# Optimization experiments

Measured on AMD Instinct MI355X. Metric: run time of the kernel, lower is better.

The kernel has to match this reference:

```python
import jax, jax.numpy as jnp
import numpy as np

V, E, H, T = 50000, 256, 512, 9
B, S = 128, 512
HD = H // 2  # per-direction LSTM hidden


def _lstm_dir(x, w_ih, w_hh, b_ih, b_hh):
    # x: [B,S,E]; PyTorch gate order i,f,g,o
    xg = jnp.einsum('bse,ge->bsg', x, w_ih) + b_ih + b_hh  # [B,S,4*HD]
    b = x.shape[0]
    h0 = jnp.zeros((b, HD), x.dtype)
    c0 = jnp.zeros((b, HD), x.dtype)

    def step(carry, xt):
        h, c = carry
        g = xt + h @ w_hh.T
        i, f, gg, o = jnp.split(g, 4, axis=-1)
        c = jax.nn.sigmoid(f) * c + jax.nn.sigmoid(i) * jnp.tanh(gg)
        h = jax.nn.sigmoid(o) * jnp.tanh(c)
        return (h, c), h

    _, hs = jax.lax.scan(step, (h0, c0), jnp.swapaxes(xg, 0, 1))
    return jnp.swapaxes(hs, 0, 1)  # [B,S,HD]


def _crf_llh(emissions, y, mask, start_trans, end_trans, trans):
    # emissions [B,S,T], y [B,S] int, mask [B,S] bool -> scalar sum LLH
    em = jnp.swapaxes(emissions, 0, 1)  # [S,B,T]
    ys = jnp.swapaxes(y, 0, 1)          # [S,B]
    mf = jnp.swapaxes(mask, 0, 1).astype(emissions.dtype)  # [S,B]
    b = emissions.shape[0]
    bidx = jnp.arange(b)

    # --- numerator: gold path score ---
    score0 = start_trans[ys[0]] + em[0, bidx, ys[0]]

    def num_step(carry, inp):
        score, yp = carry
        e_t, y_t, m_t = inp
        s = trans[yp, y_t] + e_t[bidx, y_t]
        score = score + s * m_t
        yp = jnp.where(m_t > 0, y_t, yp)
        return (score, yp), None

    (score, ylast), _ = jax.lax.scan(num_step, (score0, ys[0]),
                                     (em[1:], ys[1:], mf[1:]))
    numerator = score + end_trans[ylast]

    # --- denominator: forward algorithm ---
    alpha0 = start_trans + em[0]  # [B,T]

    def den_step(alpha, inp):
        e_t, m_t = inp
        nxt = jax.nn.logsumexp(alpha[:, :, None] + trans[None] + e_t[:, None, :], axis=1)
        return jnp.where(m_t[:, None] > 0, nxt, alpha), None

    alpha, _ = jax.lax.scan(den_step, alpha0, (em[1:], mf[1:]))
    denominator = jax.nn.logsumexp(alpha + end_trans, axis=1)
    return jnp.sum(numerator - denominator)


def setup_inputs() -> dict:
    key = jax.random.key(0)
    ks = jax.random.split(key, 16)
    X = jax.random.randint(ks[0], (B, S), 0, V)
    y = jax.random.randint(ks[1], (B, S), 0, T)
    lengths = jax.random.randint(ks[2], (B,), S // 2, S + 1)
    mask = jnp.arange(S)[None, :] < lengths[:, None]  # contiguous, mask[:,0]=True
    s = 0.1
    emb = jax.random.normal(ks[3], (V, E), jnp.float32)
    w_ih_f = jax.random.normal(ks[4], (4 * HD, E), jnp.float32) * s
    w_hh_f = jax.random.normal(ks[5], (4 * HD, HD), jnp.float32) * s
    b_ih_f = jnp.zeros((4 * HD,), jnp.float32)
    b_hh_f = jnp.zeros((4 * HD,), jnp.float32)
    w_ih_b = jax.random.normal(ks[6], (4 * HD, E), jnp.float32) * s
    w_hh_b = jax.random.normal(ks[7], (4 * HD, HD), jnp.float32) * s
    b_ih_b = jnp.zeros((4 * HD,), jnp.float32)
    b_hh_b = jnp.zeros((4 * HD,), jnp.float32)
    lin_w = jax.random.normal(ks[8], (T, H), jnp.float32) * s
    lin_b = jnp.zeros((T,), jnp.float32)
    start_trans = jax.random.uniform(ks[9], (T,), jnp.float32, -0.1, 0.1)
    end_trans = jax.random.uniform(ks[10], (T,), jnp.float32, -0.1, 0.1)
    trans = jax.random.uniform(ks[11], (T, T), jnp.float32, -0.1, 0.1)
    return dict(X=X, y=y, mask=mask, emb=emb,
                w_ih_f=w_ih_f, w_hh_f=w_hh_f, b_ih_f=b_ih_f, b_hh_f=b_hh_f,
                w_ih_b=w_ih_b, w_hh_b=w_hh_b, b_ih_b=b_ih_b, b_hh_b=b_hh_b,
                lin_w=lin_w, lin_b=lin_b,
                start_trans=start_trans, end_trans=end_trans, trans=trans)


def reference(X, y, mask, emb,
              w_ih_f, w_hh_f, b_ih_f, b_hh_f,
              w_ih_b, w_hh_b, b_ih_b, b_hh_b,
              lin_w, lin_b, start_trans, end_trans, trans):
    x = emb[X]  # [B,S,E]
    h_f = _lstm_dir(x, w_ih_f, w_hh_f, b_ih_f, b_hh_f)
    h_b = _lstm_dir(x[:, ::-1, :], w_ih_b, w_hh_b, b_ih_b, b_hh_b)[:, ::-1, :]
    o = jnp.concatenate([h_f, h_b], axis=-1)  # [B,S,H]
    emissions = jnp.einsum('bsh,th->bst', o, lin_w) + lin_b  # [B,S,T]
    return _crf_llh(emissions, y, mask, start_trans, end_trans, trans)
```

## Files before the change

kernel.cpp:

```cpp
#include <hip/hip_runtime.h>


typedef short v8s __attribute__((ext_vector_type(8)));
typedef float v4f __attribute__((ext_vector_type(4)));
typedef int   i4v __attribute__((ext_vector_type(4)));
typedef int   i8v __attribute__((ext_vector_type(8)));
typedef float v2f __attribute__((ext_vector_type(2)));

#define LOG2E  1.4426950408889634f
#define LOG2E2 2.8853900817779268f

__device__ __forceinline__ short f2b(float f){
  unsigned u = __float_as_uint(f);
  u = u + 0x7fffu + ((u >> 16) & 1u);
  return (short)(u >> 16);
}
__device__ __forceinline__ float b2f(short s){
  return __uint_as_float(((unsigned)(unsigned short)s) << 16);
}
__device__ __forceinline__ float rcp_(float x){ return __builtin_amdgcn_rcpf(x); }
__device__ __forceinline__ float ex2(float x){ return __builtin_amdgcn_exp2f(x); }
__device__ __forceinline__ float med3(float x, float lo, float hi){
  return __builtin_amdgcn_fmed3f(x, lo, hi);
}
__device__ __forceinline__ float selq(v4f v, int q){
  return q==0 ? v[0] : q==1 ? v[1] : q==2 ? v[2] : v[3];
}
__device__ __forceinline__ int fp4q(float v){
  int s = (v < 0.f) ? 8 : 0;
  float av = fabsf(v);
  int m;
  if(av < 0.25f) m=0; else if(av < 0.75f) m=1; else if(av < 1.25f) m=2;
  else if(av < 1.75f) m=3; else if(av < 2.5f) m=4; else if(av < 3.5f) m=5;
  else if(av < 5.f) m=6; else m=7;
  return s | m;
}

__global__ void prep_kernel(const float* wihf, const float* whhf,
                            const float* wihb, const float* whhb,
                            const float* bihf, const float* bhhf,
                            const float* bihb, const float* bhhb,
                            short* wswz, unsigned char* whh4, int2* whsc,
                            float* cb, float* em, float* outp)
{
  int gid = blockIdx.x * 256 + threadIdx.x;
  if(gid < 65536){
    int mat = gid >> 15;
    int rem = gid & 32767;
    int ct = rem >> 9;
    int kk = (rem >> 6) & 7;
    int lane = rem & 63;
    const float* src = mat ? wihb : wihf;
    int g  = ct*16 + (lane & 15);
    float fac = ((g >> 8) == 2) ? LOG2E2 : LOG2E;
    int k0 = kk*32 + (lane >> 4)*8;
    v8s o;
#pragma unroll
    for(int j=0;j<8;j++) o[j] = f2b(src[g*256 + k0 + j] * fac);
    *(v8s*)(wswz + ((long)mat << 18) + ((long)((ct*8+kk)*64 + lane) << 3)) = o;
  } else if(gid < 73728){
    int j2 = gid - 65536;
    int dir = j2 >> 12;
    int rem = j2 & 4095;
    int ct = rem >> 6;
    int lane = rem & 63;
    const float* src = dir ? whhb : whhf;
    int g = ct*16 + (lane & 15);
    float fac = ((g >> 8) == 2) ? LOG2E2 : LOG2E;
    int sc0 = 127, sc1 = 127;
#pragma unroll
    for(int half=0; half<2; half++){
      const float* s = src + g*256 + half*128 + (lane>>4)*32;
      float am = 0.f;
#pragma unroll
      for(int j=0;j<32;j++) am = fmaxf(am, fabsf(s[j]*fac));
      int e = 0;
      if(am > 0.f){
        e = (int)ceilf(log2f(am * (1.f/6.f)));
        e = e < -126 ? -126 : (e > 127 ? 127 : e);
      }
      float inv = exp2f((float)(-e)) * fac;
      i4v ov;
#pragma unroll
      for(int wi=0; wi<4; wi++){
        int word = 0;
#pragma unroll
        for(int bj=0; bj<4; bj++){
          int j0 = (wi*4 + bj)*2;
          int c0 = fp4q(s[j0]*inv), c1 = fp4q(s[j0+1]*inv);
          word |= (c0 | (c1<<4)) << (8*bj);
        }
        ov[wi] = word;
      }
      *(i4v*)(whh4 + ((long)((dir*64+ct)*2 + half) << 10) + lane*16) = ov;
      if(half == 0) sc0 = e + 127; else sc1 = e + 127;
    }
    whsc[(dir*64+ct)*64 + lane] = make_int2(sc0, sc1);
  } else if(gid >= 106496 && gid < 108544){
    int j3 = gid - 106496;
    int dir = j3 >> 10, gg = j3 & 1023;
    float fac = ((gg >> 8) == 2) ? LOG2E2 : LOG2E;
    cb[j3] = fac * (dir ? (bihb[gg] + bhhb[gg]) : (bihf[gg] + bhhf[gg]));
  }
  for(int i=gid; i<589824; i+=131072) em[i] = 0.f;
  if(gid == 0) *outp = 0.f;
}

__global__ __launch_bounds__(256,2) void xg_gemm(const int* X, const float* emb,
     const short* wswz, const float* cb, short* xg, int t_base, int CT)
{
  int dir = blockIdx.x & 1;
  int tl  = blockIdx.x >> 1;
  int rh  = blockIdx.y;
  int tg  = t_base + tl;
  int tt  = dir ? (511 - tg) : tg;
  __shared__ short a_sh[64*264];
  int tid = threadIdx.x;
  {
    int row = tid >> 2, seg = tid & 3;
    int b = rh*64 + row;
    int idx = X[b*512 + tt];
    const float* erow = emb + (long)idx*256 + seg*64;
    short* dst = a_sh + row*264 + seg*64;
#pragma unroll
    for(int c=0;c<8;c++){
      float4 f0 = ((const float4*)erow)[2*c];
      float4 f1 = ((const float4*)erow)[2*c+1];
      v8s p;
      p[0]=f2b(f0.x); p[1]=f2b(f0.y); p[2]=f2b(f0.z); p[3]=f2b(f0.w);
      p[4]=f2b(f1.x); p[5]=f2b(f1.y); p[6]=f2b(f1.z); p[7]=f2b(f1.w);
      *(v8s*)(dst + c*8) = p;
    }
  }
  __syncthreads();
  int w = tid >> 6, lane = tid & 63, lm = lane & 15, lq = lane >> 4;
  v8s A[4][8];
#pragma unroll
  for(int mt=0;mt<4;mt++)
#pragma unroll
    for(int kk=0;kk<8;kk++)
      A[mt][kk] = *(const v8s*)(a_sh + (mt*16+lm)*264 + kk*32 + lq*8);

  const short* wmat = wswz + ((long)dir << 18);
  const float* cbd  = cb + dir*1024;
  short* xgd = xg + ((long)dir*CT + tl)*131072;

  v8s Bb[2][8];
  {
    const short* bp = wmat + (long)(w*16)*4096 + lane*8;
#pragma unroll
    for(int kk=0;kk<8;kk++) Bb[0][kk] = *(const v8s*)(bp + kk*512);
  }
#pragma unroll
  for(int ci=0;ci<16;ci++){
    int cur = ci & 1;
    int ct = w*16 + ci;
    if(ci < 15){
      const short* bp = wmat + (long)(ct+1)*4096 + lane*8;
#pragma unroll
      for(int kk=0;kk<8;kk++) Bb[cur^1][kk] = *(const v8s*)(bp + kk*512);
    }
    float bias = cbd[ct*16 + lm];
    v4f acc[4];
#pragma unroll
    for(int mt=0;mt<4;mt++) acc[mt] = (v4f){bias,bias,bias,bias};
#pragma unroll
    for(int kk=0;kk<8;kk++)
#pragma unroll
      for(int mt=0;mt<4;mt++)
        acc[mt] = __builtin_amdgcn_mfma_f32_16x16x32_bf16(A[mt][kk], Bb[cur][kk], acc[mt], 0,0,0);
#pragma unroll
    for(int mt=0;mt<4;mt++){
      int r = rh*4 + mt;
      long off = (long)r*16384 + (long)(ct & 15)*1024 + (ct >> 4)*256 + lane*4;
      short4 s4;
      s4.x = f2b(acc[mt][0]); s4.y = f2b(acc[mt][1]);
      s4.z = f2b(acc[mt][2]); s4.w = f2b(acc[mt][3]);
      *(short4*)(xgd + off) = s4;
    }
  }
}

__global__ void emiss_partial(const unsigned char* hg8, const float* lin_w,
                              float* em, int t_base, int CT)
{
  int dir = blockIdx.y;
  int wv  = blockIdx.x*4 + (threadIdx.x >> 6);
  int lane = threadIdx.x & 63;
  int tl = wv >> 7, b = wv & 127;
  int s = dir ? (511 - (t_base + tl)) : (t_base + tl);
  int v = *(const int*)(hg8 + ((long)dir*CT + tl)*32768 + b*256 + lane*4);
  v2f lo = __builtin_amdgcn_cvt_pk_f32_fp8(v, 0);
  v2f hi = __builtin_amdgcn_cvt_pk_f32_fp8(v, 1);
  float x0 = lo[0], x1 = lo[1], x2 = hi[0], x3 = hi[1];
  const float* wbase = lin_w + dir*256 + lane*4;
  float part[9];
#pragma unroll
  for(int j=0;j<9;j++){
    float4 wf = *(const float4*)(wbase + j*512);
    part[j] = x0*wf.x + x1*wf.y + x2*wf.z + x3*wf.w;
  }
#pragma unroll
  for(int j=0;j<9;j++){
    float vv = part[j];
#pragma unroll
    for(int off=32; off>0; off>>=1) vv += __shfl_down(vv, off);
    if(lane == 0) em[((long)b*512 + s)*9 + j] += vv;
  }
}

__global__ __launch_bounds__(1024,1) void fused_step(
     const int* __restrict__ X, const float* __restrict__ emb,
     const short* __restrict__ wswz, const float* __restrict__ cb,
     const short* __restrict__ xg_rd, short* __restrict__ xg_wr,
     const unsigned char* __restrict__ whh4, const int2* __restrict__ whsc,
     unsigned char* __restrict__ hg_wr, const unsigned char* __restrict__ hg_rd,
     float* __restrict__ c_state, unsigned char* __restrict__ h_state,
     const float* __restrict__ lin_w, float* __restrict__ em,
     int first, int CT, int tb_gemm, int tb_emiss, int ng)
{
  __shared__ __align__(16) short a_sh4[4*16*264];
  int bx = blockIdx.x;
  int tid = threadIdx.x;

  if(bx < 64){
    unsigned char* hbuf = (unsigned char*)a_sh4;
    int wg = bx;
    int dir = wg >> 5, rg = wg & 31;
    int w = tid >> 6, lane = tid & 63, lm = lane & 15, lq = lane >> 4;
    int lr = lm & 3;

    i8v B8[4][2];
#pragma unroll
    for(int grp=0; grp<4; grp++)
#pragma unroll
      for(int half=0; half<2; half++){
        i4v b = *(const i4v*)(whh4 + ((long)((dir*64 + grp*16 + w)*2 + half) << 10) + lane*16);
        i8v t;
#pragma unroll
        for(int j=0;j<4;j++){ t[j] = b[j]; t[4+j] = 0; }
        B8[grp][half] = t;
      }
    int scp[2];
#pragma unroll
    for(int gp=0; gp<2; gp++){
      int2 s0 = whsc[(dir*64 + (2*gp+0)*16 + w)*64 + lane];
      int2 s1 = whsc[(dir*64 + (2*gp+1)*16 + w)*64 + lane];
      scp[gp] = (s0.x & 255) | ((s0.y & 255) << 8) | ((s1.x & 255) << 16) | ((s1.y & 255) << 24);
    }

    for(int i=tid; i<8704; i+=1024) hbuf[i] = 0;
    float c = first ? 0.f : c_state[wg*1024 + tid];
    __syncthreads();
    if(!first && tid < 256){
      int row = tid >> 6, col = tid & 63;
      *(int*)(hbuf + row*272 + col*4) = *(const int*)(h_state + wg*1024 + row*256 + col*4);
    }
    __syncthreads();

    const short* __restrict__ xbase =
        xg_rd + ((long)dir*CT)*131072 + (long)(rg >> 2)*16384 + w*1024 + ((rg & 3)*16 + lm)*4;
    int hrow = tid >> 6, hcol = tid & 63;
    unsigned char* __restrict__ houtb =
        hg_wr + (long)dir*CT*32768 + (rg*4 + hrow)*256 + hcol*4;

    short4 xa0 = *(const short4*)(xbase);
    short4 xa1 = *(const short4*)(xbase + 256);
    short4 xa2 = *(const short4*)(xbase + 512);
    short4 xa3 = *(const short4*)(xbase + 768);

    int p = 0;
    for(int tl=0; tl<CT; tl++){
      const short* __restrict__ xn = xbase + 131072;
      short4 xn0 = *(const short4*)(xn);
      short4 xn1 = *(const short4*)(xn + 256);
      short4 xn2 = *(const short4*)(xn + 512);
      short4 xn3 = *(const short4*)(xn + 768);

      const unsigned char* hb = hbuf + p*4352;
      union { i8v v8; i4v v4[2]; } a0, a1;
      a0.v4[0] = *(const i4v*)(hb + lr*272 + lq*32);
      a0.v4[1] = *(const i4v*)(hb + lr*272 + lq*32 + 16);
      a1.v4[0] = *(const i4v*)(hb + lr*272 + 128 + lq*32);
      a1.v4[1] = *(const i4v*)(hb + lr*272 + 128 + lq*32 + 16);

      v4f acc[4];
      acc[0] = (v4f){b2f(xa0.x), b2f(xa0.y), b2f(xa0.z), b2f(xa0.w)};
      acc[1] = (v4f){b2f(xa1.x), b2f(xa1.y), b2f(xa1.z), b2f(xa1.w)};
      acc[2] = (v4f){b2f(xa2.x), b2f(xa2.y), b2f(xa2.z), b2f(xa2.w)};
      acc[3] = (v4f){b2f(xa3.x), b2f(xa3.y), b2f(xa3.z), b2f(xa3.w)};

      acc[0] = __builtin_amdgcn_mfma_scale_f32_16x16x128_f8f6f4(a0.v8, B8[0][0], acc[0], 0, 4, 0, 127, 0, scp[0]);
      acc[0] = __builtin_amdgcn_mfma_scale_f32_16x16x128_f8f6f4(a1.v8, B8[0][1], acc[0], 0, 4, 0, 127, 1, scp[0]);
      acc[1] = __builtin_amdgcn_mfma_scale_f32_16x16x128_f8f6f4(a0.v8, B8[1][0], acc[1], 0, 4, 0, 127, 2, scp[0]);
      acc[1] = __builtin_amdgcn_mfma_scale_f32_16x16x128_f8f6f4(a1.v8, B8[1][1], acc[1], 0, 4, 0, 127, 3, scp[0]);
      acc[2] = __builtin_amdgcn_mfma_scale_f32_16x16x128_f8f6f4(a0.v8, B8[2][0], acc[2], 0, 4, 0, 127, 0, scp[1]);
      acc[2] = __builtin_amdgcn_mfma_scale_f32_16x16x128_f8f6f4(a1.v8, B8[2][1], acc[2], 0, 4, 0, 127, 1, scp[1]);
      acc[3] = __builtin_amdgcn_mfma_scale_f32_16x16x128_f8f6f4(a0.v8, B8[3][0], acc[3], 0, 4, 0, 127, 2, scp[1]);
      acc[3] = __builtin_amdgcn_mfma_scale_f32_16x16x128_f8f6f4(a1.v8, B8[3][1], acc[3], 0, 4, 0, 127, 3, scp[1]);

      float g0 = selq(acc[0], lq);
      float g1 = selq(acc[1], lq);
      float g2 = selq(acc[2], lq);
      float g3 = selq(acc[3], lq);

      unsigned char* hnew = hbuf + (p^1)*4352;
      {
        float ig = g0;
        float fg = g1;
        float gg = med3(g2, -40.f, 40.f);
        float og = g3;
        float t  = ex2(gg);
        float a  = ex2(-ig);
        float b  = ex2(-fg);
        float u  = ex2(-og);
        float term = (t - 1.f) * rcp_((1.f + a)*(1.f + t));
        float cn = c*rcp_(1.f + b) + term;
        c = cn;
        float cc = med3(cn*LOG2E2, -40.f, 40.f);
        float d2 = ex2(cc);
        float hv = (d2 - 1.f)*rcp_((1.f + u)*(1.f + d2));
        int packed = __builtin_amdgcn_cvt_pk_fp8_f32(hv, hv, 0, 0);
        hnew[lq*272 + 16*w + lm] = (unsigned char)(packed & 0xff);
      }
      __syncthreads();
      if(tid < 256)
        *(int*)houtb = *(const int*)(hnew + hrow*272 + hcol*4);
      houtb += 32768;
      xbase += 131072;
      xa0 = xn0; xa1 = xn1; xa2 = xn2; xa3 = xn3;
      p ^= 1;
    }
    {
      const unsigned char* hb = hbuf + p*4352;
      if(tid < 256)
        *(int*)(h_state + wg*1024 + hrow*256 + hcol*4) = *(const int*)(hb + hrow*272 + hcol*4);
      c_state[wg*1024 + tid] = c;
    }

  } else if(bx < 64 + ng){
    int q = tid >> 8;
    int t256 = tid & 255;
    int u = (bx - 64)*4 + q;
    int dir = u & 1;
    int v = u >> 1;
    int tl = v % CT;
    int rgh = v / CT;
    int tg = tb_gemm + tl;
    int tt = dir ? (511 - tg) : tg;
    short* a_shq = a_sh4 + q*4224;
    int w2 = t256 >> 6, lane = t256 & 63, lm = lane & 15, lq = lane >> 4;
    const short* wmat = wswz + ((long)dir << 18);
    const float* cbd  = cb + dir*1024;
    short* xgd = xg_wr + ((long)dir*CT + tl)*131072;

    for(int it=0; it<4; it++){
      int rg = rgh*4 + it;
      {
        int row = t256 >> 4, seg = t256 & 15;
        int b = rg*16 + row;
        int idx = X[b*512 + tt];
        const float* erow = emb + (long)idx*256 + seg*16;
        float4 f0 = ((const float4*)erow)[0];
        float4 f1 = ((const float4*)erow)[1];
        float4 f2 = ((const float4*)erow)[2];
        float4 f3 = ((const float4*)erow)[3];
        v8s p0, p1;
        p0[0]=f2b(f0.x); p0[1]=f2b(f0.y); p0[2]=f2b(f0.z); p0[3]=f2b(f0.w);
        p0[4]=f2b(f1.x); p0[5]=f2b(f1.y); p0[6]=f2b(f1.z); p0[7]=f2b(f1.w);
        p1[0]=f2b(f2.x); p1[1]=f2b(f2.y); p1[2]=f2b(f2.z); p1[3]=f2b(f2.w);
        p1[4]=f2b(f3.x); p1[5]=f2b(f3.y); p1[6]=f2b(f3.z); p1[7]=f2b(f3.w);
        *(v8s*)(a_shq + row*264 + seg*16) = p0;
        *(v8s*)(a_shq + row*264 + seg*16 + 8) = p1;
      }
      __syncthreads();
      v8s A[8];
#pragma unroll
      for(int kk=0;kk<8;kk++)
        A[kk] = *(const v8s*)(a_shq + lm*264 + kk*32 + lq*8);

#pragma unroll 1
      for(int ci=0; ci<16; ci++){
        int ct = w2*16 + ci;
        const short* bp = wmat + (long)ct*4096 + lane*8;
        v8s Bb[8];
#pragma unroll
        for(int kk=0;kk<8;kk++) Bb[kk] = *(const v8s*)(bp + kk*512);
        float bias = cbd[ct*16 + lm];
        v4f acc = (v4f){bias,bias,bias,bias};
#pragma unroll
        for(int kk=0;kk<8;kk++)
          acc = __builtin_amdgcn_mfma_f32_16x16x32_bf16(A[kk], Bb[kk], acc, 0,0,0);
        long off = (long)rg*16384 + (long)(ct & 15)*1024 + (ct >> 4)*256 + lane*4;
        short4 s4;
        s4.x = f2b(acc[0]); s4.y = f2b(acc[1]);
        s4.z = f2b(acc[2]); s4.w = f2b(acc[3]);
        *(short4*)(xgd + off) = s4;
      }
      __syncthreads();
    }

  } else {
    int uv = (bx - 64 - ng)*16 + (tid >> 6);
    int lane = tid & 63;
    int per = CT << 7;
    int dir = (uv >= per) ? 1 : 0;
    int rest = uv - (dir ? per : 0);
    int tl = rest >> 7, b = rest & 127;
    int s = dir ? (511 - (tb_emiss + tl)) : (tb_emiss + tl);
    int v = *(const int*)(hg_rd + ((long)dir*CT + tl)*32768 + b*256 + lane*4);
    v2f lo = __builtin_amdgcn_cvt_pk_f32_fp8(v, 0);
    v2f hi = __builtin_amdgcn_cvt_pk_f32_fp8(v, 1);
    float x0 = lo[0], x1 = lo[1], x2 = hi[0], x3 = hi[1];
    const float* wbase = lin_w + dir*256 + lane*4;
    float part[9];
#pragma unroll
    for(int j=0;j<9;j++){
      float4 wf = *(const float4*)(wbase + j*512);
      part[j] = x0*wf.x + x1*wf.y + x2*wf.z + x3*wf.w;
    }
#pragma unroll
    for(int j=0;j<9;j++){
      float vv = part[j];
#pragma unroll
      for(int off=32; off>0; off>>=1) vv += __shfl_down(vv, off);
      if(lane == 0) em[((long)b*512 + s)*9 + j] += vv;
    }
  }
}

__global__ __launch_bounds__(64) void crf_kernel(
                           const float* em, const int* y, const unsigned char* maskb,
                           const float* st, const float* en, const float* tr,
                           const float* lin_b, float* out)
{
  __shared__ __align__(16) float ems[4608];
  int b = blockIdx.x;
  int lane = threadIdx.x;

  {
    const float4* src = (const float4*)(em + (long)b*4608);
    float4* dst = (float4*)ems;
    for(int i = lane; i < 1152; i += 64) dst[i] = src[i];
  }

  bool isb = (maskb[1] != 0);
  int len = 0;
  for(int k=lane; k<512; k+=64){
    unsigned char mv = isb ? maskb[b*512 + k] : maskb[((long)(b*512 + k))*4];
    len += (mv != 0);
  }
#pragma unroll
  for(int off=32; off>0; off>>=1) len += __shfl_xor(len, off);

  __syncthreads();

  const int* yb = y + b*512;
  float np = 0.f;
  for(int t=lane; t<512; t+=64){
    if(t >= 1 && t < len){
      int yp = yb[t-1], yt = yb[t];
      np += tr[yp*9 + yt] + ems[t*9 + yt] + lin_b[yt];
    }
  }
#pragma unroll
  for(int off=32; off>0; off>>=1) np += __shfl_xor(np, off);

  int j = lane;
  float alpha = -1e30f;
  float trc[9];
  float lb = (j < 9) ? lin_b[j] : 0.f;
  if(j < 9){
    alpha = st[j] + ems[j] + lb;
#pragma unroll
    for(int i=0;i<9;i++) trc[i] = tr[i*9 + j];
  }
  for(int t=1; t<len; t++){
    float av[9];
#pragma unroll
    for(int i=0;i<9;i++) av[i] = __shfl(alpha, i);
    if(j < 9){
      float m = av[0] + trc[0];
#pragma unroll
      for(int i=1;i<9;i++) m = fmaxf(m, av[i] + trc[i]);
      float ssum = 0.f;
#pragma unroll
      for(int i=0;i<9;i++) ssum += __expf(av[i] + trc[i] - m);
      alpha = m + __logf(ssum) + ems[t*9 + j] + lb;
    }
  }
  float aj = (j < 9) ? (alpha + en[j]) : -1e30f;
  float mm = aj;
#pragma unroll
  for(int off=32; off>0; off>>=1) mm = fmaxf(mm, __shfl_xor(mm, off));
  float ee = (j < 9) ? __expf(aj - mm) : 0.f;
#pragma unroll
  for(int off=32; off>0; off>>=1) ee += __shfl_xor(ee, off);
  float den = mm + __logf(ee);
  if(lane == 0){
    int y0 = yb[0];
    float num = np + st[y0] + ems[y0] + lin_b[y0] + en[yb[len-1]];
    atomicAdd(out, num - den);
  }
}

extern "C" void kernel_launch(void* const* d_in, const int* in_sizes, int n_in,
                              void* d_out, int out_size, void* d_ws, size_t ws_size,
                              hipStream_t stream)
{
  (void)in_sizes; (void)n_in; (void)out_size;
  const int*   X    = (const int*)d_in[0];
  const int*   y    = (const int*)d_in[1];
  const unsigned char* maskb = (const unsigned char*)d_in[2];
  const float* emb  = (const float*)d_in[3];
  const float* wihf = (const float*)d_in[4];
  const float* whhf = (const float*)d_in[5];
  const float* bihf = (const float*)d_in[6];
  const float* bhhf = (const float*)d_in[7];
  const float* wihb = (const float*)d_in[8];
  const float* whhb = (const float*)d_in[9];
  const float* bihb = (const float*)d_in[10];
  const float* bhhb = (const float*)d_in[11];
  const float* lin_w= (const float*)d_in[12];
  const float* lin_b= (const float*)d_in[13];
  const float* st   = (const float*)d_in[14];
  const float* en   = (const float*)d_in[15];
  const float* tr   = (const float*)d_in[16];

  const long FIXED = 4595712L;
  long CT = 128;
  while (CT > 16 && FIXED + 2*CT*589824L > (long)ws_size) CT >>= 1;
  int NC = (int)(512 / CT);

  char* ws = (char*)d_ws;
  short*         wswz = (short*)(ws);
  unsigned char* whh4 = (unsigned char*)(ws + 1572864L);
  int2*          whsc = (int2*)(ws + 1835008L);
  float*         cb   = (float*)(ws + 1900544L);
  float*         cst  = (float*)(ws + 1908736L);
  unsigned char* hst  = (unsigned char*)(ws + 2170880L);
  float*         em   = (float*)(ws + 2236416L);
  short*         xg0  = (short*)(ws + FIXED);
  short*         xg1  = xg0 + CT*262144;
  unsigned char* hg0  = (unsigned char*)(ws + FIXED + 2*CT*524288L);
  unsigned char* hg1  = hg0 + CT*65536;

  prep_kernel<<<512, 256, 0, stream>>>(wihf, whhf, wihb, whhb,
                                       bihf, bhhf, bihb, bhhb,
                                       wswz, whh4, whsc, cb, em, (float*)d_out);
  xg_gemm<<<dim3(2*(int)CT, 2), 256, 0, stream>>>(X, emb, wswz, cb, xg0, 0, (int)CT);

  for(int k=0; k<NC; k++){
    short* xr = (k&1) ? xg1 : xg0;
    short* xw = (k&1) ? xg0 : xg1;
    unsigned char* hw = (k&1) ? hg1 : hg0;
    unsigned char* hr = (k&1) ? hg0 : hg1;
    int ng = (k+1 < NC) ? (int)CT : 0;
    int ne = (k >= 1)   ? (int)(16*CT) : 0;
    fused_step<<<64 + ng + ne, 1024, 0, stream>>>(
        X, emb, wswz, cb, xr, xw, whh4, whsc, hw, hr, cst, hst, lin_w, em,
        (k==0) ? 1 : 0, (int)CT, (k+1)*(int)CT, (k-1)*(int)CT, ng);
  }
  unsigned char* hlast = ((NC-1)&1) ? hg1 : hg0;
  emiss_partial<<<dim3(32*(int)CT, 2), 256, 0, stream>>>(hlast, lin_w, em, (NC-1)*(int)CT, (int)CT);
  crf_kernel<<<128, 64, 0, stream>>>(em, y, maskb, st, en, tr, lin_b, (float*)d_out);
}
```

Measured before the change: 816.2 us.

## Rewrite CRF forward pass as per-thread exp-domain matvec with precomputed exp(trans)

Splits the CRF kernel into numerator blocks and two denominator blocks, in which each thread runs the whole forward algorithm for one batch row. The denominator works in the exp domain: exp(trans + lin_b) is precomputed once in prep, so each step is one max, 9 exp2, an 81-FMA matvec and 9 log2, with no cross-lane shuffles and no shared-memory staging. It aims to shorten the serial dependency chain of the latency-bound recurrence. In exchange, each thread always runs all 511 steps and masks them instead of stopping at its length, emission reads are strided per thread, and the exp-domain form trades some numerical headroom for speed.

```diff
diff --git a/kernel.cpp b/kernel.cpp
--- a/kernel.cpp
+++ b/kernel.cpp
@@ -9,6 +9,7 @@
 
 #define LOG2E  1.4426950408889634f
 #define LOG2E2 2.8853900817779268f
+#define LN2    0.6931471805599453f
 
 __device__ __forceinline__ short f2b(float f){
   unsigned u = __float_as_uint(f);
@@ -40,8 +41,9 @@
                             const float* wihb, const float* whhb,
                             const float* bihf, const float* bhhf,
                             const float* bihb, const float* bhhb,
+                            const float* tr, const float* linb,
                             short* wswz, unsigned char* whh4, int2* whsc,
-                            float* cb, float* em, float* outp)
+                            float* cb, float* emt, float* em, float* outp)
 {
   int gid = blockIdx.x * 256 + threadIdx.x;
   if(gid < 65536){
@@ -101,6 +103,9 @@
     int dir = j3 >> 10, gg = j3 & 1023;
     float fac = ((gg >> 8) == 2) ? LOG2E2 : LOG2E;
     cb[j3] = fac * (dir ? (bihb[gg] + bhhb[gg]) : (bihf[gg] + bhhf[gg]));
+  } else if(gid >= 108544 && gid < 108625){
+    int g = gid - 108544;
+    emt[g] = expf(tr[g] + linb[g % 9]);
   }
   for(int i=gid; i<589824; i+=131072) em[i] = 0.f;
   if(gid == 0) *outp = 0.f;
@@ -432,75 +437,108 @@
 __global__ __launch_bounds__(64) void crf_kernel(
                            const float* em, const int* y, const unsigned char* maskb,
                            const float* st, const float* en, const float* tr,
-                           const float* lin_b, float* out)
+                           const float* lin_b, const float* emt, float* out)
 {
-  __shared__ __align__(16) float ems[4608];
-  int b = blockIdx.x;
+  int bx = blockIdx.x;
   int lane = threadIdx.x;
-
-  {
-    const float4* src = (const float4*)(em + (long)b*4608);
-    float4* dst = (float4*)ems;
-    for(int i = lane; i < 1152; i += 64) dst[i] = src[i];
-  }
-
   bool isb = (maskb[1] != 0);
-  int len = 0;
-  for(int k=lane; k<512; k+=64){
-    unsigned char mv = isb ? maskb[b*512 + k] : maskb[((long)(b*512 + k))*4];
-    len += (mv != 0);
-  }
-#pragma unroll
-  for(int off=32; off>0; off>>=1) len += __shfl_xor(len, off);
-
-  __syncthreads();
-
-  const int* yb = y + b*512;
-  float np = 0.f;
-  for(int t=lane; t<512; t+=64){
-    if(t >= 1 && t < len){
-      int yp = yb[t-1], yt = yb[t];
-      np += tr[yp*9 + yt] + ems[t*9 + yt] + lin_b[yt];
-    }
-  }
-#pragma unroll
-  for(int off=32; off>0; off>>=1) np += __shfl_xor(np, off);
-
-  int j = lane;
-  float alpha = -1e30f;
-  float trc[9];
-  float lb = (j < 9) ? lin_b[j] : 0.f;
-  if(j < 9){
-    alpha = st[j] + ems[j] + lb;
-#pragma unroll
-    for(int i=0;i<9;i++) trc[i] = tr[i*9 + j];
-  }
-  for(int t=1; t<len; t++){
-    float av[9];
-#pragma unroll
-    for(int i=0;i<9;i++) av[i] = __shfl(alpha, i);
-    if(j < 9){
-      float m = av[0] + trc[0];
-#pragma unroll
-      for(int i=1;i<9;i++) m = fmaxf(m, av[i] + trc[i]);
-      float ssum = 0.f;
-#pragma unroll
-      for(int i=0;i<9;i++) ssum += __expf(av[i] + trc[i] - m);
-      alpha = m + __logf(ssum) + ems[t*9 + j] + lb;
-    }
-  }
-  float aj = (j < 9) ? (alpha + en[j]) : -1e30f;
-  float mm = aj;
-#pragma unroll
-  for(int off=32; off>0; off>>=1) mm = fmaxf(mm, __shfl_xor(mm, off));
-  float ee = (j < 9) ? __expf(aj - mm) : 0.f;
-#pragma unroll
-  for(int off=32; off>0; off>>=1) ee += __shfl_xor(ee, off);
-  float den = mm + __logf(ee);
-  if(lane == 0){
-    int y0 = yb[0];
-    float num = np + st[y0] + ems[y0] + lin_b[y0] + en[yb[len-1]];
-    atomicAdd(out, num - den);
+
+  if(bx < 128){
+    int b = bx;
+    int len = 0;
+    for(int k=lane; k<512; k+=64){
+      unsigned char mv = isb ? maskb[b*512 + k] : maskb[((long)(b*512 + k))*4];
+      len += (mv != 0);
+    }
+#pragma unroll
+    for(int off=32; off>0; off>>=1) len += __shfl_xor(len, off);
+
+    const int* yb = y + b*512;
+    float np = 0.f;
+    for(int t=lane; t<512; t+=64){
+      if(t >= 1 && t < len){
+        int yp = yb[t-1], yt = yb[t];
+        np += tr[yp*9 + yt] + em[((long)b*512 + t)*9 + yt] + lin_b[yt];
+      }
+    }
+#pragma unroll
+    for(int off=32; off>0; off>>=1) np += __shfl_xor(np, off);
+
+    if(lane == 0){
+      int y0 = yb[0];
+      float num = np + st[y0] + em[(long)b*4608 + y0] + lin_b[y0] + en[yb[len-1]];
+      atomicAdd(out, num);
+    }
+  } else {
+    int b = (bx - 128)*64 + lane;
+
+    int len = 0;
+    if(isb){
+      const i4v* row = (const i4v*)(maskb + (long)b*512);
+      for(int k=0; k<32; k++){
+        i4v v = row[k];
+        len += __popc(v[0] & 0x01010101) + __popc(v[1] & 0x01010101)
+             + __popc(v[2] & 0x01010101) + __popc(v[3] & 0x01010101);
+      }
+    } else {
+      const i4v* row = (const i4v*)(maskb + (long)b*2048);
+      for(int k=0; k<128; k++){
+        i4v v = row[k];
+        len += (v[0]!=0) + (v[1]!=0) + (v[2]!=0) + (v[3]!=0);
+      }
+    }
+
+    float M[81];
+#pragma unroll
+    for(int g=0; g<81; g++) M[g] = emt[g];
+
+    const float* emb_ = em + (long)b*4608;
+    float a[9];
+#pragma unroll
+    for(int j=0;j<9;j++) a[j] = (st[j] + lin_b[j] + emb_[j]) * LOG2E;
+
+    float emn[9];
+#pragma unroll
+    for(int j=0;j<9;j++) emn[j] = emb_[9 + j];
+
+    for(int t=1; t<512; t++){
+      float emc[9];
+#pragma unroll
+      for(int j=0;j<9;j++) emc[j] = emn[j];
+#pragma unroll
+      for(int j=0;j<9;j++) emn[j] = emb_[(t+1)*9 + j];
+
+      float m = fmaxf(fmaxf(fmaxf(fmaxf(a[0],a[1]),fmaxf(a[2],a[3])),
+                            fmaxf(fmaxf(a[4],a[5]),fmaxf(a[6],a[7]))), a[8]);
+      float e[9];
+#pragma unroll
+      for(int i=0;i<9;i++) e[i] = ex2(a[i] - m);
+
+      bool live = (t < len);
+#pragma unroll
+      for(int j=0;j<9;j++){
+        float s = e[0]*M[0*9+j];
+#pragma unroll
+        for(int i=1;i<9;i++) s = fmaf(e[i], M[i*9+j], s);
+        float na = fmaf(emc[j], LOG2E, m + __log2f(s));
+        a[j] = live ? na : a[j];
+      }
+    }
+
+    float ae[9];
+#pragma unroll
+    for(int j=0;j<9;j++) ae[j] = fmaf(en[j], LOG2E, a[j]);
+    float m2 = fmaxf(fmaxf(fmaxf(fmaxf(ae[0],ae[1]),fmaxf(ae[2],ae[3])),
+                           fmaxf(fmaxf(ae[4],ae[5]),fmaxf(ae[6],ae[7]))), ae[8]);
+    float ss = 0.f;
+#pragma unroll
+    for(int j=0;j<9;j++) ss += ex2(ae[j] - m2);
+    float den = LN2 * (m2 + __log2f(ss));
+
+    float v = -den;
+#pragma unroll
+    for(int off=32; off>0; off>>=1) v += __shfl_xor(v, off);
+    if(lane == 0) atomicAdd(out, v);
   }
 }
 
@@ -534,6 +572,7 @@
 
   char* ws = (char*)d_ws;
   short*         wswz = (short*)(ws);
+  float*         emt  = (float*)(ws + 1048576L);
   unsigned char* whh4 = (unsigned char*)(ws + 1572864L);
   int2*          whsc = (int2*)(ws + 1835008L);
   float*         cb   = (float*)(ws + 1900544L);
@@ -546,8 +585,8 @@
   unsigned char* hg1  = hg0 + CT*65536;
 
   prep_kernel<<<512, 256, 0, stream>>>(wihf, whhf, wihb, whhb,
-                                       bihf, bhhf, bihb, bhhb,
-                                       wswz, whh4, whsc, cb, em, (float*)d_out);
+                                       bihf, bhhf, bihb, bhhb, tr, lin_b,
+                                       wswz, whh4, whsc, cb, emt, em, (float*)d_out);
   xg_gemm<<<dim3(2*(int)CT, 2), 256, 0, stream>>>(X, emb, wswz, cb, xg0, 0, (int)CT);
 
   for(int k=0; k<NC; k++){
@@ -563,5 +602,5 @@
   }
   unsigned char* hlast = ((NC-1)&1) ? hg1 : hg0;
   emiss_partial<<<dim3(32*(int)CT, 2), 256, 0, stream>>>(hlast, lin_w, em, (NC-1)*(int)CT, (int)CT);
-  crf_kernel<<<128, 64, 0, stream>>>(em, y, maskb, st, en, tr, lin_b, (float*)d_out);
-}
+  crf_kernel<<<130, 64, 0, stream>>>(em, y, maskb, st, en, tr, lin_b, emt, (float*)d_out);
+}
```

Result: slower. 873.6 us (+7.0%).
